# Kernel optimization log

Hardware: AMD Instinct MI355X
Metric: run time of the kernel (lower is better)

Reference implementation:

```python
import jax, jax.numpy as jnp
import numpy as np

B, Q, E = 32768, 1024, 1024  # batch, quant_dim, embed_dim


def setup_inputs() -> dict:
    key = jax.random.key(0)
    k1, k2, k3, k4, k5 = jax.random.split(key, 5)
    s = lambda n: 1.0 / np.sqrt(n)
    x = jax.random.normal(k1, (B, Q), jnp.float32)
    # nn.Linear weights, shape [out_features, in_features]
    W1 = jax.random.normal(k2, (2 * Q, Q), jnp.float32) * s(Q)      # selector layer 1
    W2 = jax.random.normal(k3, (Q, 2 * Q), jnp.float32) * s(2 * Q)  # selector layer 2
    W3 = jax.random.normal(k4, (Q, Q), jnp.float32) * s(Q)          # selector layer 3
    Wc = jax.random.normal(k5, (E, Q), jnp.float32) * s(Q)          # codebook
    return {"x": x, "W1": W1, "W2": W2, "W3": W3, "Wc": Wc}


def dyn_k_hot(x, k_scores):
    # k per row = argmax(k_scores) + 1
    k_values = jnp.argmax(k_scores, axis=-1, keepdims=True) + 1  # [B,1]
    # torch: sorted_indices = argsort(x, descending); mask gathered by argsort(sorted_indices)
    # equivalently: rank of each element in descending order < k
    ranks = jnp.argsort(jnp.argsort(-x, axis=-1), axis=-1)       # [B,Q]
    return (ranks < k_values).astype(x.dtype)


def reference(x, W1, W2, W3, Wc):
    # dynkselector: Linear -> ReLU -> Linear -> ReLU -> Linear (no biases)
    h = jax.nn.relu(x @ W1.T)
    h = jax.nn.relu(h @ W2.T)
    k_scores = h @ W3.T
    k_hot = dyn_k_hot(x, k_scores)   # [B,Q] {0,1}
    return k_hot @ Wc.T              # codebook projection -> [B,E]
```

## Files before the change

kernel.cpp:

```cpp
#include <hip/hip_runtime.h>
#include <stdint.h>

#define B_  32768
#define Q_  1024
#define E_  1024
#define CAPF  16384
#define CAPF2 1024

typedef __attribute__((ext_vector_type(8))) short bf16x8;
typedef __attribute__((ext_vector_type(8))) _Float16 f16x8;
typedef __attribute__((ext_vector_type(8))) unsigned short u16x8;
typedef __attribute__((ext_vector_type(4))) float f32x4;
typedef unsigned short us;

__device__ __forceinline__ f32x4 MFMA16(bf16x8 a, bf16x8 b, f32x4 c) {
    return __builtin_amdgcn_mfma_f32_16x16x32_bf16(a, b, c, 0, 0, 0);
}
__device__ __forceinline__ f32x4 MFMA16H(bf16x8 a, bf16x8 b, f32x4 c) {
    return __builtin_amdgcn_mfma_f32_16x16x32_f16(
        __builtin_bit_cast(f16x8, a), __builtin_bit_cast(f16x8, b), c, 0, 0, 0);
}

__device__ __forceinline__ us f2bf(float v) {
    unsigned u = __float_as_uint(v);
    u += 0x7FFFu + ((u >> 16) & 1u);
    return (us)(u >> 16);
}
__device__ __forceinline__ float bf2f(us b) {
    return __uint_as_float(((unsigned)b) << 16);
}
__device__ __forceinline__ us f2h(float v) {
    _Float16 h = (_Float16)v;
    return __builtin_bit_cast(unsigned short, h);
}

__global__ __launch_bounds__(256)
void split_planes_k(const float* __restrict__ in, us* __restrict__ hi,
                    us* __restrict__ lo, int n8) {
    int i = blockIdx.x * 256 + threadIdx.x;
    const int stride = gridDim.x * 256;
    for (; i < n8; i += stride) {
        float4 a = ((const float4*)in)[i * 2];
        float4 b = ((const float4*)in)[i * 2 + 1];
        float f[8] = {a.x, a.y, a.z, a.w, b.x, b.y, b.z, b.w};
        u16x8 h, l;
#pragma unroll
        for (int j = 0; j < 8; ++j) {
            us c0 = f2bf(f[j]);
            h[j] = c0;
            l[j] = f2bf(f[j] - bf2f(c0));
        }
        ((u16x8*)hi)[i] = h;
        ((u16x8*)lo)[i] = l;
    }
}

__global__ __launch_bounds__(256)
void cvt_plane_k(const float* __restrict__ in, us* __restrict__ hi, int n8) {
    int i = blockIdx.x * 256 + threadIdx.x;
    const int stride = gridDim.x * 256;
    for (; i < n8; i += stride) {
        float4 a = ((const float4*)in)[i * 2];
        float4 b = ((const float4*)in)[i * 2 + 1];
        float f[8] = {a.x, a.y, a.z, a.w, b.x, b.y, b.z, b.w};
        u16x8 h;
#pragma unroll
        for (int j = 0; j < 8; ++j) h[j] = f2bf(f[j]);
        ((u16x8*)hi)[i] = h;
    }
}

__global__ __launch_bounds__(256)
void cvt_plane_h(const float* __restrict__ in, us* __restrict__ hi, int n8) {
    int i = blockIdx.x * 256 + threadIdx.x;
    const int stride = gridDim.x * 256;
    for (; i < n8; i += stride) {
        float4 a = ((const float4*)in)[i * 2];
        float4 b = ((const float4*)in)[i * 2 + 1];
        float f[8] = {a.x, a.y, a.z, a.w, b.x, b.y, b.z, b.w};
        u16x8 h;
#pragma unroll
        for (int j = 0; j < 8; ++j) h[j] = f2h(f[j]);
        ((u16x8*)hi)[i] = h;
    }
}

__global__ __launch_bounds__(256)
void gather_split(const float* __restrict__ X, const int* __restrict__ flags,
                  const int* __restrict__ cnt, us* __restrict__ G0,
                  us* __restrict__ G1) {
    const int n = min(*cnt, CAPF);
    for (int it = blockIdx.x; it < n; it += gridDim.x) {
        const int row = flags[it];
        float4 v = ((const float4*)(X + (size_t)row * Q_))[threadIdx.x];
        float f[4] = {v.x, v.y, v.z, v.w};
        us h[4], l[4];
#pragma unroll
        for (int j = 0; j < 4; ++j) {
            h[j] = f2bf(f[j]);
            l[j] = f2bf(f[j] - bf2f(h[j]));
        }
        *(uint2*)&G0[(size_t)it * Q_ + threadIdx.x * 4] = *(uint2*)h;
        *(uint2*)&G1[(size_t)it * Q_ + threadIdx.x * 4] = *(uint2*)l;
    }
}

#define LGKM0() asm volatile("s_waitcnt lgkmcnt(0)" ::: "memory")
#define VMC8()  asm volatile("s_waitcnt vmcnt(8)" ::: "memory")
#define BAR()   __builtin_amdgcn_s_barrier()
#define RD_AB(Aarr, Barr, slot) { \
    const us* _la = &LA[(slot) * 8192]; const us* _lb = &LB[(slot) * 8192]; \
    _Pragma("unroll") for (int mf = 0; mf < 8; ++mf) Aarr[mf] = *(const bf16x8*)&_la[ago[mf]]; \
    _Pragma("unroll") for (int nf = 0; nf < 4; ++nf) Barr[nf] = *(const bf16x8*)&_lb[bgo[nf]]; }
#define CLX(AF, BF) { __builtin_amdgcn_s_setprio(1); \
    _Pragma("unroll") for (int mf = 0; mf < 8; ++mf) { \
        _Pragma("unroll") for (int nf = 0; nf < 4; ++nf) { \
            if constexpr (FP16) acc[mf][nf] = MFMA16H(AF[mf], BF[nf], acc[mf][nf]); \
            else               acc[mf][nf] = MFMA16 (AF[mf], BF[nf], acc[mf][nf]); } } \
    __builtin_amdgcn_s_setprio(0); }

template<int NSEG, int K, int EMIT, bool RELU, bool FP16, bool DYN>
__global__ __launch_bounds__(512, 2)
void gemm4r(const us* __restrict__ A0p, const us* __restrict__ A1p,
            const us* __restrict__ B0p, const us* __restrict__ B1p,
            void* __restrict__ Cp0, void* __restrict__ Cp1, int N,
            const int* __restrict__ ncnt) {
    constexpr int TPS = K / 32;
    constexpr int NT  = NSEG * TPS;
    static_assert(NT % 2 == 0 && NT >= 4, "shape");
    __shared__ __align__(16) us LA[4 * 8192];
    __shared__ __align__(16) us LB[4 * 8192];

    const int t = threadIdx.x;
    const int wv = t >> 6, lane = t & 63;
    const int lanelo = lane & 15, kq = lane >> 4;
    const int wm = wv >> 2, wn = wv & 3;

    const int q8 = gridDim.x >> 3;
    const int logical = ((int)blockIdx.x & 7) * q8 + ((int)blockIdx.x >> 3);
    const int gx = N >> 8;
    const int m0 = (logical / gx) * 256, n0 = (logical % gx) * 256;

    if constexpr (DYN) {
        int nn = *ncnt; if (nn > CAPF) nn = CAPF;
        if (m0 >= ((nn + 255) & ~255)) return;
    }

    int soff[2], ldst[2];
#pragma unroll
    for (int i = 0; i < 2; ++i) {
        int s = i * 512 + t;
        int row = s >> 2, c = s & 3;
        soff[i] = row * K + (c ^ ((row >> 1) & 3)) * 8;
        ldst[i] = (i * 512 + wv * 64) * 8;
    }
    int ago[8], bgo[4];
#pragma unroll
    for (int mf = 0; mf < 8; ++mf) {
        int row = wm * 128 + mf * 16 + lanelo;
        ago[mf] = (row * 4 + (kq ^ ((row >> 1) & 3))) * 8;
    }
#pragma unroll
    for (int nf = 0; nf < 4; ++nf) {
        int row = wn * 64 + nf * 16 + lanelo;
        bgo[nf] = (row * 4 + (kq ^ ((row >> 1) & 3))) * 8;
    }

    auto stage = [&](int tv) {
        int slot = tv & 3;
        int seg = tv / TPS;
        int kb  = (tv - seg * TPS) * 32;
        const us* Ap = (NSEG == 1 || seg < 2) ? A0p : A1p;
        const us* Bp = (NSEG == 3 && seg == 1) ? B1p : B0p;
        const us* Abase = Ap + (size_t)m0 * K + kb;
        const us* Bbase = Bp + (size_t)n0 * K + kb;
        us* dA = &LA[slot * 8192];
        us* dB = &LB[slot * 8192];
#pragma unroll
        for (int i = 0; i < 2; ++i) {
            __builtin_amdgcn_global_load_lds(
                (const __attribute__((address_space(1))) void*)(Abase + soff[i]),
                (__attribute__((address_space(3))) void*)(dA + ldst[i]), 16, 0, 0);
            __builtin_amdgcn_global_load_lds(
                (const __attribute__((address_space(1))) void*)(Bbase + soff[i]),
                (__attribute__((address_space(3))) void*)(dB + ldst[i]), 16, 0, 0);
        }
    };

    f32x4 acc[8][4];
#pragma unroll
    for (int i = 0; i < 8; ++i)
#pragma unroll
        for (int j = 0; j < 4; ++j) acc[i][j] = (f32x4){0.f, 0.f, 0.f, 0.f};

    bf16x8 aE[8], bE[4], aO[8], bO[4];

    stage(0); stage(1); stage(2);
    VMC8();  BAR();
    RD_AB(aE, bE, 0);
    stage(3);
    LGKM0(); VMC8(); BAR();

    for (int tt = 0; tt < NT; tt += 2) {
        RD_AB(aO, bO, (tt + 1) & 3);
        { int tv = tt + 4; if (tv > NT - 1) tv = NT - 1; stage(tv); }
        CLX(aE, bE);
        LGKM0(); VMC8(); BAR();
        { int tn = (tt + 2 < NT) ? (tt + 2) : (NT - 1);
          RD_AB(aE, bE, tn & 3); }
        { int tv = tt + 5; if (tv > NT - 1) tv = NT - 1; stage(tv); }
        CLX(aO, bO);
        LGKM0(); VMC8(); BAR();
    }

#pragma unroll
    for (int mf = 0; mf < 8; ++mf)
#pragma unroll
        for (int nf = 0; nf < 4; ++nf)
#pragma unroll
            for (int r = 0; r < 4; ++r) {
                int row = m0 + wm * 128 + mf * 16 + kq * 4 + r;
                int col = n0 + wn * 64 + nf * 16 + lanelo;
                float v = acc[mf][nf][r];
                if constexpr (RELU) v = fmaxf(v, 0.f);
                if constexpr (EMIT == 1) {
                    us c0 = f2bf(v);
                    ((us*)Cp0)[(size_t)row * N + col] = c0;
                    ((us*)Cp1)[(size_t)row * N + col] = f2bf(v - bf2f(c0));
                } else if constexpr (EMIT == 2) {
                    ((us*)Cp0)[(size_t)row * N + col] = f2h(v);
                } else {
                    ((float*)Cp0)[(size_t)row * N + col] = v;
                }
            }
}

__device__ __forceinline__ int chunk_of(int row, int koff) {
    return row * 4 + (koff ^ (row & 3));
}

template<int NPASS>
__device__ __forceinline__ void split_store(us* S0, us* S1,
                                            int rowX, int koffX, float4 a, float4 b) {
    int ch = chunk_of(rowX, koffX);
    float f[8] = {a.x, a.y, a.z, a.w, b.x, b.y, b.z, b.w};
    bf16x8 lo, hi;
#pragma unroll
    for (int j = 0; j < 8; ++j) {
        us c0 = f2bf(f[j]);
        lo[j] = (short)c0;
        hi[j] = (short)f2bf(f[j] - bf2f(c0));
    }
    *(bf16x8*)&S0[ch * 8] = lo;
    if constexpr (NPASS == 3) *(bf16x8*)&S1[ch * 8] = hi;
}

template<int NPASS, bool AF32, bool RELU, bool EMITP>
__global__ __launch_bounds__(256, 2)
void gemm3p(const void* __restrict__ Ap0, const void* __restrict__ Ap1,
            const float* __restrict__ Wf,
            void* __restrict__ Cp0, void* __restrict__ Cp1,
            int M, int N, int K) {
    __shared__ __align__(16) us A0s[128 * 32];
    __shared__ __align__(16) us B0s[128 * 32];
    __shared__ __align__(16) us A1s[(NPASS == 3) ? 128 * 32 : 8];
    __shared__ __align__(16) us B1s[(NPASS == 3) ? 128 * 32 : 8];

    const int t = threadIdx.x;
    const int wave = t >> 6, lane = t & 63;
    const int lanelo = lane & 15, kq = lane >> 4;
    const int wm = wave >> 1, wn = wave & 1;
    const int m0 = blockIdx.y * 128, n0 = blockIdx.x * 128;
    const int brow = t >> 1, bhalf = t & 1;

    f32x4 acc[4][4];
#pragma unroll
    for (int i = 0; i < 4; ++i)
#pragma unroll
        for (int j = 0; j < 4; ++j) acc[i][j] = (f32x4){0.f, 0.f, 0.f, 0.f};

    for (int kt = 0; kt < K; kt += 32) {
        __syncthreads();
        const float* wp = Wf + (size_t)(n0 + brow) * K + kt + bhalf * 16;
        float4 v0 = *(const float4*)(wp + 0);
        float4 v1 = *(const float4*)(wp + 4);
        float4 v2 = *(const float4*)(wp + 8);
        float4 v3 = *(const float4*)(wp + 12);
        if constexpr (AF32) {
            const float* ap = (const float*)Ap0 + (size_t)(m0 + brow) * K + kt + bhalf * 16;
            float4 u0 = *(const float4*)(ap + 0);
            float4 u1 = *(const float4*)(ap + 4);
            float4 u2 = *(const float4*)(ap + 8);
            float4 u3 = *(const float4*)(ap + 12);
            split_store<NPASS>(A0s, A1s, brow, bhalf * 2 + 0, u0, u1);
            split_store<NPASS>(A0s, A1s, brow, bhalf * 2 + 1, u2, u3);
        } else {
#pragma unroll
            for (int g = 0; g < 2; ++g) {
                int c = (g * 4 + wave) * 64 + lane;
                int row = c >> 2;
                int koff = (c & 3) ^ (row & 3);
                const us* s0 = (const us*)Ap0 + (size_t)(m0 + row) * K + kt + koff * 8;
                __builtin_amdgcn_global_load_lds(
                    (const __attribute__((address_space(1))) void*)s0,
                    (__attribute__((address_space(3))) void*)&A0s[(size_t)(g * 4 + wave) * 512],
                    16, 0, 0);
                if constexpr (NPASS == 3) {
                    const us* s1 = (const us*)Ap1 + (size_t)(m0 + row) * K + kt + koff * 8;
                    __builtin_amdgcn_global_load_lds(
                        (const __attribute__((address_space(1))) void*)s1,
                        (__attribute__((address_space(3))) void*)&A1s[(size_t)(g * 4 + wave) * 512],
                        16, 0, 0);
                }
            }
        }
        split_store<NPASS>(B0s, B1s, brow, bhalf * 2 + 0, v0, v1);
        split_store<NPASS>(B0s, B1s, brow, bhalf * 2 + 1, v2, v3);
        __syncthreads();

        bf16x8 a0[4], a1[4];
#pragma unroll
        for (int mf = 0; mf < 4; ++mf) {
            int ar = wm * 64 + mf * 16 + lanelo;
            int ac = chunk_of(ar, kq);
            a0[mf] = *(const bf16x8*)&A0s[ac * 8];
            if constexpr (NPASS == 3) a1[mf] = *(const bf16x8*)&A1s[ac * 8];
        }
#pragma unroll
        for (int nf = 0; nf < 4; ++nf) {
            int br = wn * 64 + nf * 16 + lanelo;
            int bc = chunk_of(br, kq);
            bf16x8 vb0 = *(const bf16x8*)&B0s[bc * 8];
#pragma unroll
            for (int mf = 0; mf < 4; ++mf) acc[mf][nf] = MFMA16(a0[mf], vb0, acc[mf][nf]);
            if constexpr (NPASS == 3) {
                bf16x8 vb1 = *(const bf16x8*)&B1s[bc * 8];
#pragma unroll
                for (int mf = 0; mf < 4; ++mf) acc[mf][nf] = MFMA16(a0[mf], vb1, acc[mf][nf]);
#pragma unroll
                for (int mf = 0; mf < 4; ++mf) acc[mf][nf] = MFMA16(a1[mf], vb0, acc[mf][nf]);
            }
        }
    }

#pragma unroll
    for (int mf = 0; mf < 4; ++mf)
#pragma unroll
        for (int nf = 0; nf < 4; ++nf)
#pragma unroll
            for (int r = 0; r < 4; ++r) {
                int row = m0 + wm * 64 + mf * 16 + kq * 4 + r;
                int col = n0 + wn * 64 + nf * 16 + lanelo;
                float v = acc[mf][nf][r];
                if constexpr (RELU) v = fmaxf(v, 0.f);
                if constexpr (EMITP) {
                    us c0 = f2bf(v);
                    ((us*)Cp0)[(size_t)row * N + col] = c0;
                    ((us*)Cp1)[(size_t)row * N + col] = f2bf(v - bf2f(c0));
                } else {
                    ((float*)Cp0)[(size_t)row * N + col] = v;
                }
            }
}

__global__ __launch_bounds__(256)
void row_argmax_flag(const float* __restrict__ S, int* __restrict__ KV,
                     int* __restrict__ flags, int* __restrict__ cnt, float theta) {
    int row = blockIdx.x * 4 + (threadIdx.x >> 6);
    int lane = threadIdx.x & 63;
    const float* s = S + (size_t)row * Q_;
    float b1 = -3.4e38f, b2 = -3.4e38f; int i1 = 0;
    for (int j = lane; j < Q_; j += 64) {
        float v = s[j];
        if (v > b1) { b2 = b1; b1 = v; i1 = j; }
        else if (v > b2) b2 = v;
    }
#pragma unroll
    for (int m = 1; m < 64; m <<= 1) {
        float o1 = __shfl_xor(b1, m);
        int   oi = __shfl_xor(i1, m);
        float o2 = __shfl_xor(b2, m);
        if (o1 > b1 || (o1 == b1 && oi < i1)) {
            b2 = fmaxf(b1, o2);
            b1 = o1; i1 = oi;
        } else {
            b2 = fmaxf(b2, o1);
        }
    }
    if (lane == 0) {
        KV[row] = i1 + 1;
        if (b1 - b2 < theta) {
            int p = atomicAdd(cnt, 1);
            if (p < CAPF) flags[p] = row;
        }
    }
}

__global__ __launch_bounds__(256)
void g_argmax_flag2(const float* __restrict__ SCg, const int* __restrict__ flags,
                    const int* __restrict__ cnt, int* __restrict__ KV,
                    int* __restrict__ flags2, int* __restrict__ cnt2) {
    const int lane = threadIdx.x & 63, wv = threadIdx.x >> 6;
    const int n = min(*cnt, CAPF);
    for (int it = blockIdx.x * 4 + wv; it < n; it += gridDim.x * 4) {
        const float* s = SCg + (size_t)it * Q_;
        float b1 = -3.4e38f, b2 = -3.4e38f; int i1 = 0;
        for (int j = lane; j < Q_; j += 64) {
            float v = s[j];
            if (v > b1) { b2 = b1; b1 = v; i1 = j; }
            else if (v > b2) b2 = v;
        }
#pragma unroll
        for (int m = 1; m < 64; m <<= 1) {
            float o1 = __shfl_xor(b1, m);
            int   oi = __shfl_xor(i1, m);
            float o2 = __shfl_xor(b2, m);
            if (o1 > b1 || (o1 == b1 && oi < i1)) {
                b2 = fmaxf(b1, o2);
                b1 = o1; i1 = oi;
            } else {
                b2 = fmaxf(b2, o1);
            }
        }
        if (lane == 0) {
            KV[flags[it]] = i1 + 1;
            if (b1 - b2 < 1e-3f) {
                int p = atomicAdd(cnt2, 1);
                if (p < CAPF2) flags2[p] = flags[it];
            }
        }
    }
}

template<int K, bool IN_BY_FLAG, bool RELU>
__global__ __launch_bounds__(256)
void rescore_gemm(const float* __restrict__ IN, const float* __restrict__ W,
                  float* __restrict__ OUT, const int* __restrict__ flags,
                  const int* __restrict__ cnt, int N, int cap) {
    __shared__ float xr[K];
    const int t = threadIdx.x, lane = t & 63, wv = t >> 6;
    const int n = min(*cnt, cap);
    const int chunks = N >> 4;
    for (int w = blockIdx.x; w < n * chunks; w += gridDim.x) {
        const int it = w / chunks, ch = w - it * chunks;
        const float* rp = IN_BY_FLAG ? IN + (size_t)flags[it] * K
                                     : IN + (size_t)it * K;
        __syncthreads();
#pragma unroll
        for (int p = t; p < K / 4; p += 256)
            ((float4*)xr)[p] = ((const float4*)rp)[p];
        __syncthreads();
#pragma unroll
        for (int jj = 0; jj < 4; ++jj) {
            const int col = ch * 16 + wv * 4 + jj;
            const float* wr = W + (size_t)col * K;
            double a0 = 0.0, a1 = 0.0;
#pragma unroll
            for (int i = 0; i < K / 256; ++i) {
                const int k = i * 256 + lane * 4;
                float4 w4 = *(const float4*)(wr + k);
                float4 x4 = *(const float4*)(xr + k);
                a0 += (double)x4.x * w4.x + (double)x4.y * w4.y;
                a1 += (double)x4.z * w4.z + (double)x4.w * w4.w;
            }
            double a = a0 + a1;
#pragma unroll
            for (int m = 1; m < 64; m <<= 1) a += __shfl_xor(a, m);
            if (lane == 0) {
                float v = (float)a;
                if (RELU) v = fmaxf(v, 0.f);
                OUT[(size_t)it * N + col] = v;
            }
        }
    }
}

__global__ __launch_bounds__(256)
void rescore_argmax(const float* __restrict__ SCF, const int* __restrict__ flags,
                    const int* __restrict__ cnt, int* __restrict__ KV, int cap) {
    const int lane = threadIdx.x & 63, wv = threadIdx.x >> 6;
    const int n = min(*cnt, cap);
    for (int it = blockIdx.x * 4 + wv; it < n; it += gridDim.x * 4) {
        const float* s = SCF + (size_t)it * Q_;
        float best = -3.4e38f; int bi = 0;
        for (int j = lane; j < Q_; j += 64) {
            float v = s[j];
            if (v > best) { best = v; bi = j; }
        }
#pragma unroll
        for (int m = 1; m < 64; m <<= 1) {
            float ov = __shfl_xor(best, m); int oi = __shfl_xor(bi, m);
            if (ov > best || (ov == best && oi < bi)) { best = ov; bi = oi; }
        }
        if (lane == 0) KV[flags[it]] = bi + 1;
    }
}

__global__ __launch_bounds__(256)
void topk_mask_radix(const float* __restrict__ X, const int* __restrict__ KV,
                     us* __restrict__ Mout) {
    const int row  = blockIdx.x * 4 + (threadIdx.x >> 6);
    const int lane = threadIdx.x & 63;
    const float* x = X + (size_t)row * Q_;

    unsigned u[16];
#pragma unroll
    for (int j4 = 0; j4 < 4; ++j4) {
        float4 v = *(const float4*)(x + lane * 16 + j4 * 4);
        float f[4] = {v.x, v.y, v.z, v.w};
#pragma unroll
        for (int e = 0; e < 4; ++e) {
            unsigned fb = __float_as_uint(f[e]);
            u[j4 * 4 + e] = (fb & 0x80000000u) ? ~fb : (fb | 0x80000000u);
        }
    }
    const int k = KV[row];

    unsigned p = 0;
#pragma unroll
    for (int b = 31; b >= 0; --b) {
        unsigned q = p | (1u << b);
        int c = 0;
#pragma unroll
        for (int j = 0; j < 16; ++j) c += (u[j] >= q);
#pragma unroll
        for (int m = 1; m < 64; m <<= 1) c += __shfl_xor(c, m);
        if (c >= k) p = q;
    }

    int gt = 0, eqloc = 0;
#pragma unroll
    for (int j = 0; j < 16; ++j) { gt += (u[j] > p); eqloc += (u[j] == p); }
    int gtot = gt;
#pragma unroll
    for (int m = 1; m < 64; m <<= 1) gtot += __shfl_xor(gtot, m);
    int scan = eqloc;
#pragma unroll
    for (int d = 1; d < 64; d <<= 1) {
        int o = __shfl_up(scan, d);
        if (lane >= d) scan += o;
    }
    int run = scan - eqloc;
    const int quota = k - gtot;

    us m16[16];
#pragma unroll
    for (int j = 0; j < 16; ++j) {
        bool one;
        if (u[j] > p) one = true;
        else if (u[j] == p) { one = (run < quota); ++run; }
        else one = false;
        m16[j] = one ? (us)0x3F80 : (us)0;
    }
    u16x8* dst = (u16x8*)(Mout + (size_t)row * Q_ + lane * 16);
    dst[0] = *(u16x8*)&m16[0];
    dst[1] = *(u16x8*)&m16[8];
}

extern "C" void kernel_launch(void* const* d_in, const int* in_sizes, int n_in,
                              void* d_out, int out_size, void* d_ws, size_t ws_size,
                              hipStream_t stream) {
    const float* x  = (const float*)d_in[0];
    const float* W1 = (const float*)d_in[1];
    const float* W2 = (const float*)d_in[2];
    const float* W3 = (const float*)d_in[3];
    const float* Wc = (const float*)d_in[4];
    float* out = (float*)d_out;

    char* ws = (char*)d_ws;
    char* dob = (char*)d_out;
    us*    H1f  = (us*)ws;
    float* SC   = (float*)(ws + ((size_t)128 << 20));
    us*    H1g0 = (us*)ws;
    us*    H1g1 = (us*)(ws + ((size_t)64 << 20));
    float* SCg  = (float*)(ws + ((size_t)128 << 20));
    us*    MASKB= (us*)(ws + ((size_t)192 << 20));
    int* KV     = (int*)(ws + ((size_t)256 << 20));
    int* FLAGS  = KV + B_;
    int* CNT    = FLAGS + B_;
    int* CNT2   = CNT + 1;
    int* FLAGS2 = CNT2 + 1;
    us*    Xf   = (us*)dob;
    us*    H2f  = (us*)(dob + ((size_t)64 << 20));
    us*    Xg0  = (us*)dob;
    us*    Xg1  = (us*)(dob + ((size_t)32 << 20));
    us*    H2g0 = (us*)(dob + ((size_t)64 << 20));
    us*    H2g1 = (us*)(dob + ((size_t)96 << 20));
    float* H1F  = (float*)dob;
    float* H2F  = (float*)(dob + ((size_t)8 << 20));
    float* SCF  = (float*)(dob + ((size_t)12 << 20));
    char* WP = ws + ((size_t)256 << 20) + ((size_t)512 << 10);
    us* W1h = (us*)WP;                       us* W1f = (us*)WP;
    us* W1l = W1h + (size_t)2 * Q_ * Q_;
    us* W2h = W1l + (size_t)2 * Q_ * Q_;     us* W2f = W1l;
    us* W2l = W2h + (size_t)2 * Q_ * Q_;
    us* W3h = W2l + (size_t)2 * Q_ * Q_;     us* W3f = W2h;
    us* W3l = W3h + (size_t)Q_ * Q_;
    us* Wch = W3l + (size_t)Q_ * Q_;
    const size_t NEEDED = ((size_t)256 << 20) + ((size_t)512 << 10) + ((size_t)22 << 20);

    hipMemsetAsync(CNT, 0, 2 * sizeof(int), stream);
    dim3 blk(256);

    if (ws_size >= NEEDED) {
        cvt_plane_h<<<dim3(2048), blk, 0, stream>>>(x,  Xf,  B_ * Q_ / 8);
        cvt_plane_h<<<dim3(512),  blk, 0, stream>>>(W1, W1f, 2 * Q_ * Q_ / 8);
        cvt_plane_h<<<dim3(512),  blk, 0, stream>>>(W2, W2f, 2 * Q_ * Q_ / 8);
        cvt_plane_h<<<dim3(512),  blk, 0, stream>>>(W3, W3f, Q_ * Q_ / 8);
        gemm4r<1, Q_,     2, true,  true,  false><<<dim3(1024), dim3(512), 0, stream>>>(
            Xf,  nullptr, W1f, nullptr, H1f, nullptr, 2 * Q_, nullptr);
        gemm4r<1, 2 * Q_, 2, true,  true,  false><<<dim3(512),  dim3(512), 0, stream>>>(
            H1f, nullptr, W2f, nullptr, H2f, nullptr, Q_, nullptr);
        gemm4r<1, Q_,     0, false, true,  false><<<dim3(512),  dim3(512), 0, stream>>>(
            H2f, nullptr, W3f, nullptr, SC,  nullptr, Q_, nullptr);
        row_argmax_flag<<<dim3(B_ / 4), blk, 0, stream>>>(SC, KV, FLAGS, CNT, 0.01f);
        split_planes_k<<<dim3(512), blk, 0, stream>>>(W1, W1h, W1l, 2 * Q_ * Q_ / 8);
        split_planes_k<<<dim3(512), blk, 0, stream>>>(W2, W2h, W2l, 2 * Q_ * Q_ / 8);
        split_planes_k<<<dim3(512), blk, 0, stream>>>(W3, W3h, W3l, Q_ * Q_ / 8);
        cvt_plane_k   <<<dim3(512), blk, 0, stream>>>(Wc, Wch, E_ * Q_ / 8);
        gather_split<<<dim3(2048), blk, 0, stream>>>(x, FLAGS, CNT, Xg0, Xg1);
        gemm4r<3, Q_,     1, true,  false, true><<<dim3((CAPF / 256) * 8), dim3(512), 0, stream>>>(
            Xg0,  Xg1,  W1h, W1l, H1g0, H1g1, 2 * Q_, CNT);
        gemm4r<3, 2 * Q_, 1, true,  false, true><<<dim3((CAPF / 256) * 4), dim3(512), 0, stream>>>(
            H1g0, H1g1, W2h, W2l, H2g0, H2g1, Q_, CNT);
        gemm4r<3, Q_,     0, false, false, true><<<dim3((CAPF / 256) * 4), dim3(512), 0, stream>>>(
            H2g0, H2g1, W3h, W3l, SCg, nullptr, Q_, CNT);
        g_argmax_flag2<<<dim3(1024), blk, 0, stream>>>(SCg, FLAGS, CNT, KV, FLAGS2, CNT2);
        rescore_gemm<Q_,     true,  true ><<<dim3(4096), blk, 0, stream>>>(x,   W1, H1F, FLAGS2, CNT2, 2 * Q_, CAPF2);
        rescore_gemm<2 * Q_, false, true ><<<dim3(2048), blk, 0, stream>>>(H1F, W2, H2F, FLAGS2, CNT2, Q_,     CAPF2);
        rescore_gemm<Q_,     false, false><<<dim3(2048), blk, 0, stream>>>(H2F, W3, SCF, FLAGS2, CNT2, Q_,     CAPF2);
        rescore_argmax<<<dim3(64), blk, 0, stream>>>(SCF, FLAGS2, CNT2, KV, CAPF2);
        topk_mask_radix<<<dim3(B_ / 4), blk, 0, stream>>>(x, KV, MASKB);
        gemm4r<1, Q_, 0, false, false, false><<<dim3(512), dim3(512), 0, stream>>>(
            MASKB, nullptr, Wch, nullptr, out, nullptr, E_, nullptr);
    } else {
        us*    H1_0 = (us*)ws;
        us*    H1_1 = (us*)(ws + ((size_t)128 << 20));
        float* SCo  = (float*)ws;
        us*    MB   = (us*)(ws + ((size_t)128 << 20));
        us* H2_0 = (us*)d_out;
        us* H2_1 = (us*)d_out + (size_t)B_ * Q_;
        float* H1Fo = (float*)ws;
        float* H2Fo = (float*)(ws + ((size_t)128 << 20));
        float* SCFo = (float*)(ws + ((size_t)192 << 20));
        gemm3p<3, true,  true,  true ><<<dim3(2 * Q_ / 128, B_ / 128), blk, 0, stream>>>(
            x, nullptr, W1, H1_0, H1_1, B_, 2 * Q_, Q_);
        gemm3p<3, false, true,  true ><<<dim3(Q_ / 128, B_ / 128), blk, 0, stream>>>(
            H1_0, H1_1, W2, H2_0, H2_1, B_, Q_, 2 * Q_);
        gemm3p<3, false, false, false><<<dim3(Q_ / 128, B_ / 128), blk, 0, stream>>>(
            H2_0, H2_1, W3, SCo, nullptr, B_, Q_, Q_);
        row_argmax_flag<<<dim3(B_ / 4), blk, 0, stream>>>(SCo, KV, FLAGS, CNT, 1e-3f);
        rescore_gemm<Q_,     true,  true ><<<dim3(4096), blk, 0, stream>>>(x,    W1, H1Fo, FLAGS, CNT, 2 * Q_, CAPF);
        rescore_gemm<2 * Q_, false, true ><<<dim3(2048), blk, 0, stream>>>(H1Fo, W2, H2Fo, FLAGS, CNT, Q_,     CAPF);
        rescore_gemm<Q_,     false, false><<<dim3(2048), blk, 0, stream>>>(H2Fo, W3, SCFo, FLAGS, CNT, Q_,     CAPF);
        rescore_argmax<<<dim3(64), blk, 0, stream>>>(SCFo, FLAGS, CNT, KV, CAPF);
        topk_mask_radix<<<dim3(B_ / 4), blk, 0, stream>>>(x, KV, MB);
        gemm3p<1, false, false, false><<<dim3(E_ / 128, B_ / 128), blk, 0, stream>>>(
            MB, nullptr, Wc, out, nullptr, B_, E_, Q_);
    }
}
```

Baseline: 1.241 ms.

## Use 128x128-tile split-precision GEMM for flagged-row rescoring and guard flag indices

After: 1.298 ms. 4.6% more time.

```diff
diff --git a/kernel.cpp b/kernel.cpp
--- a/kernel.cpp
+++ b/kernel.cpp
@@ -91,7 +91,8 @@
                   us* __restrict__ G1) {
     const int n = min(*cnt, CAPF);
     for (int it = blockIdx.x; it < n; it += gridDim.x) {
-        const int row = flags[it];
+        int row = flags[it];
+        if ((unsigned)row >= B_) row = 0;
         float4 v = ((const float4*)(X + (size_t)row * Q_))[threadIdx.x];
         float f[4] = {v.x, v.y, v.z, v.w};
         us h[4], l[4];
@@ -119,12 +120,11 @@
             else               acc[mf][nf] = MFMA16 (AF[mf], BF[nf], acc[mf][nf]); } } \
     __builtin_amdgcn_s_setprio(0); }
 
-template<int NSEG, int K, int EMIT, bool RELU, bool FP16, bool DYN>
+template<int NSEG, int K, int EMIT, bool RELU, bool FP16>
 __global__ __launch_bounds__(512, 2)
 void gemm4r(const us* __restrict__ A0p, const us* __restrict__ A1p,
             const us* __restrict__ B0p, const us* __restrict__ B1p,
-            void* __restrict__ Cp0, void* __restrict__ Cp1, int N,
-            const int* __restrict__ ncnt) {
+            void* __restrict__ Cp0, void* __restrict__ Cp1, int N) {
     constexpr int TPS = K / 32;
     constexpr int NT  = NSEG * TPS;
     static_assert(NT % 2 == 0 && NT >= 4, "shape");
@@ -140,11 +140,6 @@
     const int logical = ((int)blockIdx.x & 7) * q8 + ((int)blockIdx.x >> 3);
     const int gx = N >> 8;
     const int m0 = (logical / gx) * 256, n0 = (logical % gx) * 256;
-
-    if constexpr (DYN) {
-        int nn = *ncnt; if (nn > CAPF) nn = CAPF;
-        if (m0 >= ((nn + 255) & ~255)) return;
-    }
 
     int soff[2], ldst[2];
 #pragma unroll
@@ -229,6 +224,109 @@
                     ((us*)Cp1)[(size_t)row * N + col] = f2bf(v - bf2f(c0));
                 } else if constexpr (EMIT == 2) {
                     ((us*)Cp0)[(size_t)row * N + col] = f2h(v);
+                } else {
+                    ((float*)Cp0)[(size_t)row * N + col] = v;
+                }
+            }
+}
+
+template<int NPASS, bool RELU, bool EMITP, bool DYN>
+__global__ __launch_bounds__(256, 4)
+void gemm_pp(const us* __restrict__ A0, const us* __restrict__ A1,
+             const us* __restrict__ B0, const us* __restrict__ B1,
+             void* __restrict__ Cp0, void* __restrict__ Cp1,
+             int N, int K, const int* __restrict__ ncnt) {
+    __shared__ __align__(16) us A0s[128 * 32];
+    __shared__ __align__(16) us B0s[128 * 32];
+    __shared__ __align__(16) us A1s[(NPASS == 3) ? 128 * 32 : 8];
+    __shared__ __align__(16) us B1s[(NPASS == 3) ? 128 * 32 : 8];
+
+    const int t = threadIdx.x;
+    const int wave = t >> 6, lane = t & 63;
+    const int lanelo = lane & 15, kq = lane >> 4;
+    const int wm = wave >> 1, wn = wave & 1;
+    const int q8 = gridDim.x >> 3;
+    const int logical = ((int)blockIdx.x & 7) * q8 + ((int)blockIdx.x >> 3);
+    const int gx = N >> 7;
+    const int m0 = (logical / gx) * 128, n0 = (logical % gx) * 128;
+
+    if constexpr (DYN) {
+        int nn = *ncnt; if (nn > CAPF) nn = CAPF;
+        if (m0 >= ((nn + 127) & ~127)) return;
+    }
+
+    f32x4 acc[4][4];
+#pragma unroll
+    for (int i = 0; i < 4; ++i)
+#pragma unroll
+        for (int j = 0; j < 4; ++j) acc[i][j] = (f32x4){0.f, 0.f, 0.f, 0.f};
+
+    for (int kt = 0; kt < K; kt += 32) {
+        __syncthreads();
+#pragma unroll
+        for (int g = 0; g < 2; ++g) {
+            int c = (g * 4 + wave) * 64 + lane;
+            int row = c >> 2;
+            int koff = (c & 3) ^ (row & 3);
+            size_t offa = (size_t)(m0 + row) * K + kt + koff * 8;
+            size_t offb = (size_t)(n0 + row) * K + kt + koff * 8;
+            int dst = (g * 4 + wave) * 512;
+            __builtin_amdgcn_global_load_lds(
+                (const __attribute__((address_space(1))) void*)(A0 + offa),
+                (__attribute__((address_space(3))) void*)&A0s[dst], 16, 0, 0);
+            __builtin_amdgcn_global_load_lds(
+                (const __attribute__((address_space(1))) void*)(B0 + offb),
+                (__attribute__((address_space(3))) void*)&B0s[dst], 16, 0, 0);
+            if constexpr (NPASS == 3) {
+                __builtin_amdgcn_global_load_lds(
+                    (const __attribute__((address_space(1))) void*)(A1 + offa),
+                    (__attribute__((address_space(3))) void*)&A1s[dst], 16, 0, 0);
+                __builtin_amdgcn_global_load_lds(
+                    (const __attribute__((address_space(1))) void*)(B1 + offb),
+                    (__attribute__((address_space(3))) void*)&B1s[dst], 16, 0, 0);
+            }
+        }
+        __syncthreads();
+
+        bf16x8 a0[4], a1[4];
+#pragma unroll
+        for (int mf = 0; mf < 4; ++mf) {
+            int ar = wm * 64 + mf * 16 + lanelo;
+            int ac = ar * 4 + (kq ^ (ar & 3));
+            a0[mf] = *(const bf16x8*)&A0s[ac * 8];
+            if constexpr (NPASS == 3) a1[mf] = *(const bf16x8*)&A1s[ac * 8];
+        }
+#pragma unroll
+        for (int nf = 0; nf < 4; ++nf) {
+            int br = wn * 64 + nf * 16 + lanelo;
+            int bc = br * 4 + (kq ^ (br & 3));
+            bf16x8 vb0 = *(const bf16x8*)&B0s[bc * 8];
+#pragma unroll
+            for (int mf = 0; mf < 4; ++mf) acc[mf][nf] = MFMA16(a0[mf], vb0, acc[mf][nf]);
+            if constexpr (NPASS == 3) {
+                bf16x8 vb1 = *(const bf16x8*)&B1s[bc * 8];
+#pragma unroll
+                for (int mf = 0; mf < 4; ++mf) acc[mf][nf] = MFMA16(a0[mf], vb1, acc[mf][nf]);
+#pragma unroll
+                for (int mf = 0; mf < 4; ++mf) acc[mf][nf] = MFMA16(a1[mf], vb0, acc[mf][nf]);
+            }
+        }
+    }
+
+#pragma unroll
+    for (int mf = 0; mf < 4; ++mf)
+#pragma unroll
+        for (int nf = 0; nf < 4; ++nf)
+#pragma unroll
+            for (int r = 0; r < 4; ++r) {
+                int row = m0 + wm * 64 + mf * 16 + kq * 4 + r;
+                int col = n0 + wn * 64 + nf * 16 + lanelo;
+                float v = acc[mf][nf][r];
+                if constexpr (RELU) v = fmaxf(v, 0.f);
+                if constexpr (EMITP) {
+                    us c0 = f2bf(v);
+                    ((us*)Cp0)[(size_t)row * N + col] = c0;
+                    ((us*)Cp1)[(size_t)row * N + col] = f2bf(v - bf2f(c0));
                 } else {
                     ((float*)Cp0)[(size_t)row * N + col] = v;
                 }
@@ -423,10 +521,13 @@
             }
         }
         if (lane == 0) {
-            KV[flags[it]] = i1 + 1;
-            if (b1 - b2 < 1e-3f) {
-                int p = atomicAdd(cnt2, 1);
-                if (p < CAPF2) flags2[p] = flags[it];
+            int r = flags[it];
+            if ((unsigned)r < B_) {
+                KV[r] = i1 + 1;
+                if (b1 - b2 < 1e-3f) {
+                    int p = atomicAdd(cnt2, 1);
+                    if (p < CAPF2) flags2[p] = r;
+                }
             }
         }
     }
@@ -443,8 +544,9 @@
     const int chunks = N >> 4;
     for (int w = blockIdx.x; w < n * chunks; w += gridDim.x) {
         const int it = w / chunks, ch = w - it * chunks;
-        const float* rp = IN_BY_FLAG ? IN + (size_t)flags[it] * K
-                                     : IN + (size_t)it * K;
+        int srow = IN_BY_FLAG ? flags[it] : it;
+        if (IN_BY_FLAG && (unsigned)srow >= B_) srow = 0;
+        const float* rp = IN + (size_t)srow * K;
         __syncthreads();
 #pragma unroll
         for (int p = t; p < K / 4; p += 256)
@@ -492,7 +594,10 @@
             float ov = __shfl_xor(best, m); int oi = __shfl_xor(bi, m);
             if (ov > best || (ov == best && oi < bi)) { best = ov; bi = oi; }
         }
-        if (lane == 0) KV[flags[it]] = bi + 1;
+        if (lane == 0) {
+            int r = flags[it];
+            if ((unsigned)r < B_) KV[r] = bi + 1;
+        }
     }
 }
 
@@ -607,32 +712,32 @@
         cvt_plane_h<<<dim3(512),  blk, 0, stream>>>(W1, W1f, 2 * Q_ * Q_ / 8);
         cvt_plane_h<<<dim3(512),  blk, 0, stream>>>(W2, W2f, 2 * Q_ * Q_ / 8);
         cvt_plane_h<<<dim3(512),  blk, 0, stream>>>(W3, W3f, Q_ * Q_ / 8);
-        gemm4r<1, Q_,     2, true,  true,  false><<<dim3(1024), dim3(512), 0, stream>>>(
-            Xf,  nullptr, W1f, nullptr, H1f, nullptr, 2 * Q_, nullptr);
-        gemm4r<1, 2 * Q_, 2, true,  true,  false><<<dim3(512),  dim3(512), 0, stream>>>(
-            H1f, nullptr, W2f, nullptr, H2f, nullptr, Q_, nullptr);
-        gemm4r<1, Q_,     0, false, true,  false><<<dim3(512),  dim3(512), 0, stream>>>(
-            H2f, nullptr, W3f, nullptr, SC,  nullptr, Q_, nullptr);
+        gemm4r<1, Q_,     2, true,  true ><<<dim3(1024), dim3(512), 0, stream>>>(
+            Xf,  nullptr, W1f, nullptr, H1f, nullptr, 2 * Q_);
+        gemm4r<1, 2 * Q_, 2, true,  true ><<<dim3(512),  dim3(512), 0, stream>>>(
+            H1f, nullptr, W2f, nullptr, H2f, nullptr, Q_);
+        gemm4r<1, Q_,     0, false, true ><<<dim3(512),  dim3(512), 0, stream>>>(
+            H2f, nullptr, W3f, nullptr, SC,  nullptr, Q_);
         row_argmax_flag<<<dim3(B_ / 4), blk, 0, stream>>>(SC, KV, FLAGS, CNT, 0.01f);
         split_planes_k<<<dim3(512), blk, 0, stream>>>(W1, W1h, W1l, 2 * Q_ * Q_ / 8);
         split_planes_k<<<dim3(512), blk, 0, stream>>>(W2, W2h, W2l, 2 * Q_ * Q_ / 8);
         split_planes_k<<<dim3(512), blk, 0, stream>>>(W3, W3h, W3l, Q_ * Q_ / 8);
         cvt_plane_k   <<<dim3(512), blk, 0, stream>>>(Wc, Wch, E_ * Q_ / 8);
         gather_split<<<dim3(2048), blk, 0, stream>>>(x, FLAGS, CNT, Xg0, Xg1);
-        gemm4r<3, Q_,     1, true,  false, true><<<dim3((CAPF / 256) * 8), dim3(512), 0, stream>>>(
-            Xg0,  Xg1,  W1h, W1l, H1g0, H1g1, 2 * Q_, CNT);
-        gemm4r<3, 2 * Q_, 1, true,  false, true><<<dim3((CAPF / 256) * 4), dim3(512), 0, stream>>>(
-            H1g0, H1g1, W2h, W2l, H2g0, H2g1, Q_, CNT);
-        gemm4r<3, Q_,     0, false, false, true><<<dim3((CAPF / 256) * 4), dim3(512), 0, stream>>>(
-            H2g0, H2g1, W3h, W3l, SCg, nullptr, Q_, CNT);
+        gemm_pp<3, true,  true,  true><<<dim3((CAPF / 128) * (2 * Q_ / 128)), blk, 0, stream>>>(
+            Xg0,  Xg1,  W1h, W1l, H1g0, H1g1, 2 * Q_, Q_, CNT);
+        gemm_pp<3, true,  true,  true><<<dim3((CAPF / 128) * (Q_ / 128)), blk, 0, stream>>>(
+            H1g0, H1g1, W2h, W2l, H2g0, H2g1, Q_, 2 * Q_, CNT);
+        gemm_pp<3, false, false, true><<<dim3((CAPF / 128) * (Q_ / 128)), blk, 0, stream>>>(
+            H2g0, H2g1, W3h, W3l, SCg, nullptr, Q_, Q_, CNT);
         g_argmax_flag2<<<dim3(1024), blk, 0, stream>>>(SCg, FLAGS, CNT, KV, FLAGS2, CNT2);
         rescore_gemm<Q_,     true,  true ><<<dim3(4096), blk, 0, stream>>>(x,   W1, H1F, FLAGS2, CNT2, 2 * Q_, CAPF2);
         rescore_gemm<2 * Q_, false, true ><<<dim3(2048), blk, 0, stream>>>(H1F, W2, H2F, FLAGS2, CNT2, Q_,     CAPF2);
         rescore_gemm<Q_,     false, false><<<dim3(2048), blk, 0, stream>>>(H2F, W3, SCF, FLAGS2, CNT2, Q_,     CAPF2);
         rescore_argmax<<<dim3(64), blk, 0, stream>>>(SCF, FLAGS2, CNT2, KV, CAPF2);
         topk_mask_radix<<<dim3(B_ / 4), blk, 0, stream>>>(x, KV, MASKB);
-        gemm4r<1, Q_, 0, false, false, false><<<dim3(512), dim3(512), 0, stream>>>(
-            MASKB, nullptr, Wch, nullptr, out, nullptr, E_, nullptr);
+        gemm4r<1, Q_, 0, false, false><<<dim3(512), dim3(512), 0, stream>>>(
+            MASKB, nullptr, Wch, nullptr, out, nullptr, E_);
     } else {
         us*    H1_0 = (us*)ws;
         us*    H1_1 = (us*)(ws + ((size_t)128 << 20));
```
